# Performance work log

Hardware: AMD Instinct MI355X
Metric: run time of the kernel (lower is better)

Reference implementation:

```python
import jax, jax.numpy as jnp
import numpy as np

B, N, C, H = 2, 2048, 512, 8
D = C // H
SCALE = D ** (-0.5)


def setup_inputs() -> dict:
    key = jax.random.key(0)
    k1, k2, k3 = jax.random.split(key, 3)
    x = jax.random.normal(k1, (B, N, C), dtype=jnp.float32)
    qkv_w = jax.random.normal(k2, (C, 3 * C), dtype=jnp.float32) * (C ** -0.5)
    proj_w = jax.random.normal(k3, (C, C), dtype=jnp.float32) * (C ** -0.5)
    proj_b = jnp.zeros((C,), dtype=jnp.float32)
    return {"x": x, "qkv_w": qkv_w, "proj_w": proj_w, "proj_b": proj_b}


def reference(x, qkv_w, proj_w, proj_b):
    # qkv projection (no bias) -> (B, N, 3, H, D) -> (3, B, H, N, D)
    qkv = jnp.einsum('bnc,cf->bnf', x, qkv_w)
    qkv = qkv.reshape(B, N, 3, H, D).transpose(2, 0, 3, 1, 4)
    q, k, v = qkv[0], qkv[1], qkv[2]
    q = q * SCALE
    attn = jnp.einsum('bhid,bhjd->bhij', q, k)          # (B, H, N, N)
    attn = jax.nn.softmax(attn, axis=-1)
    out = jnp.einsum('bhij,bhjd->bhid', attn, v)         # (B, H, N, D)
    # Faithful to source: reshape (B,H,N,D) -> (B,N,C) WITHOUT transposing
    out = out.reshape(B, N, C)
    out = jnp.einsum('bnc,cd->bnd', out, proj_w) + proj_b
    return out
```

## Files before the change

kernel.cpp:

```cpp
#include <hip/hip_runtime.h>
#include <math.h>

constexpr int Bb = 2;
constexpr int Nn = 2048;
constexpr int Cc = 512;
constexpr int Hh = 8;
constexpr int Dd = 64;

typedef short short8 __attribute__((ext_vector_type(8)));
typedef float floatx4 __attribute__((ext_vector_type(4)));
typedef float floatx16 __attribute__((ext_vector_type(16)));

__device__ inline short8 bcs8(uint4 u) { return __builtin_bit_cast(short8, u); }
__device__ inline float4 bcf4(uint4 u) { return __builtin_bit_cast(float4, u); }

__device__ inline floatx4 mfma16(short8 a, short8 b, floatx4 c) {
    return __builtin_amdgcn_mfma_f32_16x16x32_bf16(a, b, c, 0, 0, 0);
}
__device__ inline floatx16 mfma32(short8 a, short8 b, floatx16 c) {
    return __builtin_amdgcn_mfma_f32_32x32x16_bf16(a, b, c, 0, 0, 0);
}

typedef __attribute__((address_space(1))) void gvoid;
typedef __attribute__((address_space(3))) void svoid;
__device__ inline void glds16(const void* g, void* l) {
    __builtin_amdgcn_global_load_lds((const gvoid*)g, (svoid*)l, 16, 0, 0);
}

#if __has_builtin(__builtin_amdgcn_exp2f)
#define EXP2(x) __builtin_amdgcn_exp2f(x)
#else
#define EXP2(x) __expf((x) * 0.69314718056f)
#endif

__device__ inline unsigned pk_trunc(float a, float b) {
    return __builtin_amdgcn_perm(__float_as_uint(b), __float_as_uint(a), 0x07060302u);
}
__device__ inline unsigned pk_rne(float a, float b) {
    unsigned ua = __float_as_uint(a); ua += 0x7fffu + ((ua >> 16) & 1u);
    unsigned ub = __float_as_uint(b); ub += 0x7fffu + ((ub >> 16) & 1u);
    return __builtin_amdgcn_perm(ub, ua, 0x07060302u);
}
__device__ inline unsigned short rne1(float a) {
    unsigned u = __float_as_uint(a); u += 0x7fffu + ((u >> 16) & 1u);
    return (unsigned short)(u >> 16);
}
__device__ inline float tr16(float a) {
    return __uint_as_float(__float_as_uint(a) & 0xffff0000u);
}
__device__ inline void split8(float4 A, float4 B, uint4& hi, uint4& lo) {
    hi = make_uint4(pk_trunc(A.x, A.y), pk_trunc(A.z, A.w),
                    pk_trunc(B.x, B.y), pk_trunc(B.z, B.w));
    lo = make_uint4(pk_trunc(A.x - tr16(A.x), A.y - tr16(A.y)),
                    pk_trunc(A.z - tr16(A.z), A.w - tr16(A.w)),
                    pk_trunc(B.x - tr16(B.x), B.y - tr16(B.y)),
                    pk_trunc(B.z - tr16(B.z), B.w - tr16(B.w)));
}

__global__ __launch_bounds__(256) void prep(const float* __restrict__ qkv_w,
                                            const float* __restrict__ proj_w,
                                            unsigned short* __restrict__ wqh,
                                            unsigned short* __restrict__ wql,
                                            unsigned short* __restrict__ wph,
                                            unsigned short* __restrict__ wpl)
{
    __shared__ float Tl[64][68];
    int bid = blockIdx.x;
    const float* src; unsigned short *dh, *dlo; int W, f0, k0;
    if (bid < 192) { int kt = bid / 24, ft = bid % 24; W = 1536; src = qkv_w; dh = wqh; dlo = wql; f0 = ft * 64; k0 = kt * 64; }
    else { int b2 = bid - 192; int kt = b2 / 8, ft = b2 % 8; W = 512; src = proj_w; dh = wph; dlo = wpl; f0 = ft * 64; k0 = kt * 64; }
    int t = threadIdx.x;
    {
        int kl = t >> 2, fc = (t & 3) * 16;
        const float* p = src + (size_t)(k0 + kl) * W + f0 + fc;
        #pragma unroll
        for (int i = 0; i < 4; ++i) {
            float4 v = *(const float4*)(p + i * 4);
            Tl[kl][fc + i * 4 + 0] = v.x; Tl[kl][fc + i * 4 + 1] = v.y;
            Tl[kl][fc + i * 4 + 2] = v.z; Tl[kl][fc + i * 4 + 3] = v.w;
        }
    }
    __syncthreads();
    {
        int fl = t >> 2, kc = (t & 3) * 16;
        float v[16];
        #pragma unroll
        for (int i = 0; i < 16; ++i) v[i] = Tl[kc + i][fl];
        unsigned hi[8], lo[8];
        #pragma unroll
        for (int i = 0; i < 8; ++i) {
            float a = v[2 * i], b = v[2 * i + 1];
            hi[i] = pk_trunc(a, b);
            lo[i] = pk_trunc(a - tr16(a), b - tr16(b));
        }
        unsigned short* oh = dh + (size_t)(f0 + fl) * 512 + k0 + kc;
        unsigned short* ol = dlo + (size_t)(f0 + fl) * 512 + k0 + kc;
        *(uint4*)oh = make_uint4(hi[0], hi[1], hi[2], hi[3]);
        *(uint4*)(oh + 8) = make_uint4(hi[4], hi[5], hi[6], hi[7]);
        *(uint4*)ol = make_uint4(lo[0], lo[1], lo[2], lo[3]);
        *(uint4*)(ol + 8) = make_uint4(lo[4], lo[5], lo[6], lo[7]);
    }
}

__global__ __launch_bounds__(256, 3) void gemm_qkv(const float* __restrict__ x,
                                                   const unsigned short* __restrict__ wh,
                                                   const unsigned short* __restrict__ wl,
                                                   unsigned short* __restrict__ qd,
                                                   unsigned short* __restrict__ kfrag,
                                                   unsigned short* __restrict__ vfrag)
{
    __shared__ __align__(16) char smem[49152];
    const int tid = threadIdx.x, lane = tid & 63, w = tid >> 6;
    const int l15 = lane & 15, l4 = lane >> 4;
    const int row0 = blockIdx.y * 128, col0 = blockIdx.x * 64;
    const int wm = w >> 1, wn = w & 1;

    floatx4 acc[4][2];
    #pragma unroll
    for (int i = 0; i < 4; ++i)
        #pragma unroll
        for (int j = 0; j < 2; ++j)
            #pragma unroll
            for (int r = 0; r < 4; ++r) acc[i][j][r] = 0.f;

    auto stage = [&](int k0, char* buf) {
        #pragma unroll
        for (int i = 0; i < 4; ++i) {
            int sid = w * 4 + i; int mt = sid >> 1, sub = sid & 1;
            const float* src = x + (size_t)(row0 + mt * 16 + l15) * 512 + k0 + l4 * 8 + sub * 4;
            glds16(src, buf + sid * 1024);
        }
        #pragma unroll
        for (int i = 0; i < 2; ++i) {
            int sid = w * 2 + i; int nt = sid >> 1, comp = sid & 1;
            const unsigned short* src = (comp ? wl : wh) + (size_t)(col0 + nt * 16 + l15) * 512 + k0 + l4 * 8;
            glds16(src, buf + 16384 + comp * 4096 + nt * 1024);
        }
    };

    stage(0, smem);
    for (int it = 0; it < 16; ++it) {
        __syncthreads();
        char* buf = smem + (it & 1) * 24576;
        if (it < 15) stage((it + 1) * 32, smem + ((it + 1) & 1) * 24576);
        char* Ab = buf; char* Bh = buf + 16384; char* Bl = buf + 20480;
        short8 af[4][2], bf[2][2];
        #pragma unroll
        for (int mt = 0; mt < 4; ++mt) {
            int off = (((wm * 4 + mt) * 2) << 10) + (lane << 4);
            float4 fa = bcf4(*(const uint4*)(Ab + off));
            float4 fb = bcf4(*(const uint4*)(Ab + off + 1024));
            uint4 hi, lo;
            split8(fa, fb, hi, lo);
            af[mt][0] = bcs8(hi);
            af[mt][1] = bcs8(lo);
        }
        #pragma unroll
        for (int nt = 0; nt < 2; ++nt) {
            int off = ((wn * 2 + nt) << 10) + (lane << 4);
            bf[nt][0] = bcs8(*(const uint4*)(Bh + off));
            bf[nt][1] = bcs8(*(const uint4*)(Bl + off));
        }
        #pragma unroll
        for (int mt = 0; mt < 4; ++mt)
            #pragma unroll
            for (int nt = 0; nt < 2; ++nt) {
                acc[mt][nt] = mfma16(af[mt][0], bf[nt][0], acc[mt][nt]);
                acc[mt][nt] = mfma16(af[mt][0], bf[nt][1], acc[mt][nt]);
                acc[mt][nt] = mfma16(af[mt][1], bf[nt][0], acc[mt][nt]);
            }
    }
    #pragma unroll
    for (int mt = 0; mt < 4; ++mt)
        #pragma unroll
        for (int nt = 0; nt < 2; ++nt) {
            int c = col0 + (wn * 2 + nt) * 16 + l15;
            int which = c >> 9;
            int head = (c >> 6) & 7, d = c & 63;
            int tokb = row0 + (wm * 4 + mt) * 16 + l4 * 4;
            int b = tokb >> 11, n = tokb & 2047;
            int bh = b * 8 + head;
            if (which == 0) {
                #pragma unroll
                for (int r = 0; r < 4; ++r)
                    qd[(size_t)(bh * 2048 + n + r) * 64 + d] = rne1(acc[mt][nt][r] * 0.18033688f);
            } else if (which == 1) {
                int s = d >> 4;
                size_t fb_ = ((size_t)(bh * 64 + (n >> 5)) * 4 + s) * 512 + (d & 7);
                int hl = ((d >> 3) & 1) * 32;
                #pragma unroll
                for (int r = 0; r < 4; ++r)
                    kfrag[fb_ + (size_t)(hl + ((n + r) & 31)) * 8] = rne1(acc[mt][nt][r]);
            } else {
                int j = n >> 4, mtv = d >> 5;
                uint2 pv;
                pv.x = pk_rne(acc[mt][nt][0], acc[mt][nt][1]);
                pv.y = pk_rne(acc[mt][nt][2], acc[mt][nt][3]);
                *(uint2*)&vfrag[((size_t)(bh * 128 + j) * 2 + mtv) * 512 +
                                (size_t)(((n >> 3) & 1) * 32 + (d & 31)) * 8 + (n & 7)] = pv;
            }
        }
}

__global__ __launch_bounds__(256, 4) void attn(const unsigned short* __restrict__ qd,
                                               const unsigned short* __restrict__ kfrag,
                                               const unsigned short* __restrict__ vfrag,
                                               unsigned short* __restrict__ Oh,
                                               unsigned short* __restrict__ Ol)
{
    __shared__ float Ms[2048];
    __shared__ float Ls[64];
    __shared__ float Ts[2176];

    int bid = blockIdx.x;
    int xcd = bid & 7; int rr = bid >> 3;
    int qt = rr & 63; int bhi = rr >> 6;
    int bh = (bhi << 3) | xcd;
    int tid = threadIdx.x, lane = tid & 63, kg = tid >> 6;
    int l31 = lane & 31, h = lane >> 5;

    short8 qf[4];
    #pragma unroll
    for (int s = 0; s < 4; ++s)
        qf[s] = bcs8(*(const uint4*)(qd + ((size_t)bh * 2048 + qt * 32 + l31) * 64 + s * 16 + h * 8));

    const uint4 onesu = make_uint4(0x3F803F80u, 0x3F803F80u, 0x3F803F80u, 0x3F803F80u);
    const short8 onesf = bcs8(onesu);

    floatx16 OT[2], OTl;
    #pragma unroll
    for (int i = 0; i < 2; ++i)
        #pragma unroll
        for (int r = 0; r < 16; ++r) OT[i][r] = 0.f;
    #pragma unroll
    for (int r = 0; r < 16; ++r) OTl[r] = 0.f;

    const unsigned short* kb_ = kfrag + ((size_t)(bh * 64 + kg * 16) * 4) * 512 + lane * 8;
    const unsigned short* vb_ = vfrag + ((size_t)(bh * 128 + kg * 32) * 2) * 512 + lane * 8;

    #pragma unroll
    for (int c = 0; c < 16; ++c) {
        uint4 kfu[4];
        #pragma unroll
        for (int s = 0; s < 4; ++s)
            kfu[s] = *(const uint4*)(kb_ + ((size_t)c * 4 + s) * 512);
        uint4 vfu[2][2];
        #pragma unroll
        for (int kc = 0; kc < 2; ++kc)
            #pragma unroll
            for (int mtv = 0; mtv < 2; ++mtv)
                vfu[kc][mtv] = *(const uint4*)(vb_ + ((size_t)(c * 2 + kc) * 2 + mtv) * 512);

        floatx16 st;
        #pragma unroll
        for (int r = 0; r < 16; ++r) st[r] = 0.f;
        #pragma unroll
        for (int s = 0; s < 4; ++s) st = mfma32(bcs8(kfu[s]), qf[s], st);

        unsigned P2[8];
        #pragma unroll
        for (int s2 = 0; s2 < 8; ++s2)
            P2[s2] = pk_trunc(EXP2(st[2 * s2]), EXP2(st[2 * s2 + 1]));

        #pragma unroll
        for (int kc = 0; kc < 2; ++kc) {
            unsigned X0 = P2[4 * kc + 0], X1 = P2[4 * kc + 1];
            unsigned Y0 = P2[4 * kc + 2], Y1 = P2[4 * kc + 3];
            unsigned T0 = h ? X0 : Y0;
            unsigned T1 = h ? X1 : Y1;
            unsigned To0 = __shfl_xor(T0, 32, 64);
            unsigned To1 = __shfl_xor(T1, 32, 64);
            uint4 fu;
            fu.x = h ? To0 : X0;
            fu.y = h ? To1 : X1;
            fu.z = h ? Y0 : To0;
            fu.w = h ? Y1 : To1;
            short8 pf = bcs8(fu);
            OT[0] = mfma32(bcs8(vfu[kc][0]), pf, OT[0]);
            OT[1] = mfma32(bcs8(vfu[kc][1]), pf, OT[1]);
            OTl = mfma32(onesf, pf, OTl);
        }
    }

    if (kg == 3) {
        #pragma unroll
        for (int mtv = 0; mtv < 2; ++mtv)
            #pragma unroll
            for (int r = 0; r < 16; ++r) {
                int d = mtv * 32 + (r & 3) + 8 * (r >> 2) + 4 * h;
                Ms[d * 32 + l31] = OT[mtv][r];
            }
        Ls[h * 32 + l31] = OTl[0];
    }
    __syncthreads();
    if (kg == 2) {
        #pragma unroll
        for (int mtv = 0; mtv < 2; ++mtv)
            #pragma unroll
            for (int r = 0; r < 16; ++r) {
                int d = mtv * 32 + (r & 3) + 8 * (r >> 2) + 4 * h;
                Ms[d * 32 + l31] += OT[mtv][r];
            }
        Ls[h * 32 + l31] += OTl[0];
    }
    __syncthreads();
    if (kg == 1) {
        #pragma unroll
        for (int mtv = 0; mtv < 2; ++mtv)
            #pragma unroll
            for (int r = 0; r < 16; ++r) {
                int d = mtv * 32 + (r & 3) + 8 * (r >> 2) + 4 * h;
                Ms[d * 32 + l31] += OT[mtv][r];
            }
        Ls[h * 32 + l31] += OTl[0];
    }
    __syncthreads();
    if (kg == 0) {
        #pragma unroll
        for (int mtv = 0; mtv < 2; ++mtv)
            #pragma unroll
            for (int r = 0; r < 16; ++r) {
                int d = mtv * 32 + (r & 3) + 8 * (r >> 2) + 4 * h;
                OT[mtv][r] += Ms[d * 32 + l31];
            }
        float inv = 1.f / (Ls[h * 32 + l31] + OTl[0]);
        #pragma unroll
        for (int mtv = 0; mtv < 2; ++mtv)
            #pragma unroll
            for (int r = 0; r < 16; ++r) {
                int d = mtv * 32 + (r & 3) + 8 * (r >> 2) + 4 * h;
                Ts[l31 * 68 + d] = OT[mtv][r] * inv;
            }
    }
    __syncthreads();
    {
        int q = tid >> 3, dc = (tid & 7) * 8;
        float vv[8];
        #pragma unroll
        for (int i = 0; i < 8; ++i) vv[i] = Ts[q * 68 + dc + i];
        unsigned hi[4], lo[4];
        #pragma unroll
        for (int i = 0; i < 4; ++i) {
            float a = vv[2 * i], bb = vv[2 * i + 1];
            hi[i] = pk_trunc(a, bb);
            lo[i] = pk_trunc(a - tr16(a), bb - tr16(bb));
        }
        size_t bo = ((size_t)(bh * 2048 + qt * 32 + q)) * 64 + dc;
        *(uint4*)(Oh + bo) = make_uint4(hi[0], hi[1], hi[2], hi[3]);
        *(uint4*)(Ol + bo) = make_uint4(lo[0], lo[1], lo[2], lo[3]);
    }
}

__global__ __launch_bounds__(256, 2) void gemm_proj(const unsigned short* __restrict__ Ah_g,
                                                    const unsigned short* __restrict__ Al_g,
                                                    const unsigned short* __restrict__ wh,
                                                    const unsigned short* __restrict__ wl,
                                                    const float* __restrict__ bias,
                                                    float* __restrict__ out)
{
    __shared__ __align__(16) char smem[32768];
    const int tid = threadIdx.x, lane = tid & 63, w = tid >> 6;
    const int l15 = lane & 15, l4 = lane >> 4;
    const int row0 = blockIdx.y * 64, col0 = blockIdx.x * 64;
    const int wm = w >> 1, wn = w & 1;

    floatx4 acc[2][2];
    #pragma unroll
    for (int i = 0; i < 2; ++i)
        #pragma unroll
        for (int j = 0; j < 2; ++j)
            #pragma unroll
            for (int r = 0; r < 4; ++r) acc[i][j][r] = 0.f;

    auto stage = [&](int k0, char* buf) {
        #pragma unroll
        for (int i = 0; i < 4; ++i) {
            int sid = w * 4 + i;
            if (sid < 8) {
                int mt = sid >> 1, comp = sid & 1;
                const unsigned short* src = (comp ? Al_g : Ah_g) + (size_t)(row0 + mt * 16 + l15) * 512 + k0 + l4 * 8;
                glds16(src, buf + (comp ? 4096 : 0) + mt * 1024);
            } else {
                int s2 = sid - 8; int nt = s2 >> 1, comp = s2 & 1;
                const unsigned short* src = (comp ? wl : wh) + (size_t)(col0 + nt * 16 + l15) * 512 + k0 + l4 * 8;
                glds16(src, buf + (comp ? 12288 : 8192) + nt * 1024);
            }
        }
    };

    stage(0, smem);
    for (int it = 0; it < 16; ++it) {
        __syncthreads();
        char* buf = smem + (it & 1) * 16384;
        if (it < 15) stage((it + 1) * 32, smem + ((it + 1) & 1) * 16384);
        char* Ah = buf; char* Al = buf + 4096; char* Bh = buf + 8192; char* Bl = buf + 12288;
        short8 af[2][2], bf[2][2];
        #pragma unroll
        for (int mt = 0; mt < 2; ++mt) {
            int off = ((wm * 2 + mt) << 10) + (lane << 4);
            af[mt][0] = bcs8(*(const uint4*)(Ah + off));
            af[mt][1] = bcs8(*(const uint4*)(Al + off));
        }
        #pragma unroll
        for (int nt = 0; nt < 2; ++nt) {
            int off = ((wn * 2 + nt) << 10) + (lane << 4);
            bf[nt][0] = bcs8(*(const uint4*)(Bh + off));
            bf[nt][1] = bcs8(*(const uint4*)(Bl + off));
        }
        #pragma unroll
        for (int mt = 0; mt < 2; ++mt)
            #pragma unroll
            for (int nt = 0; nt < 2; ++nt) {
                acc[mt][nt] = mfma16(af[mt][0], bf[nt][0], acc[mt][nt]);
                acc[mt][nt] = mfma16(af[mt][0], bf[nt][1], acc[mt][nt]);
                acc[mt][nt] = mfma16(af[mt][1], bf[nt][0], acc[mt][nt]);
            }
    }
    #pragma unroll
    for (int mt = 0; mt < 2; ++mt)
        #pragma unroll
        for (int nt = 0; nt < 2; ++nt) {
            int c = col0 + (wn * 2 + nt) * 16 + l15;
            float bv = bias[c];
            #pragma unroll
            for (int r = 0; r < 4; ++r) {
                int tok = row0 + (wm * 2 + mt) * 16 + l4 * 4 + r;
                out[(size_t)tok * 512 + c] = acc[mt][nt][r] + bv;
            }
        }
}

extern "C" void kernel_launch(void* const* d_in, const int* in_sizes, int n_in,
                              void* d_out, int out_size, void* d_ws, size_t ws_size,
                              hipStream_t stream)
{
    const float* x      = (const float*)d_in[0];
    const float* qkv_w  = (const float*)d_in[1];
    const float* proj_w = (const float*)d_in[2];
    const float* proj_b = (const float*)d_in[3];
    float* out = (float*)d_out;

    char* ws = (char*)d_ws;
    unsigned short* qd    = (unsigned short*)ws;
    unsigned short* kfrag = (unsigned short*)(ws + 4194304);
    unsigned short* vfrag = (unsigned short*)(ws + 8388608);
    unsigned short* wqh   = (unsigned short*)(ws + 12582912);
    unsigned short* wql   = (unsigned short*)(ws + 14155776);
    unsigned short* wph   = (unsigned short*)(ws + 15728640);
    unsigned short* wpl   = (unsigned short*)(ws + 16252928);
    unsigned short* Oh    = (unsigned short*)(ws + 16777216);
    unsigned short* Ol    = (unsigned short*)(ws + 20971520);

    prep<<<256, 256, 0, stream>>>(qkv_w, proj_w, wqh, wql, wph, wpl);
    gemm_qkv<<<dim3(24, 32), 256, 0, stream>>>(x, wqh, wql, qd, kfrag, vfrag);
    attn<<<1024, 256, 0, stream>>>(qd, kfrag, vfrag, Oh, Ol);
    gemm_proj<<<dim3(8, 64), 256, 0, stream>>>(Oh, Ol, wph, wpl, proj_b, out);
}
```

Before: 149.9 us.

## Pre-pack GEMM operands into MFMA fragment layout and drop LDS staging

The prep kernel now also splits x into bf16 hi/lo and writes x, both weight matrices, and the attention output into a fragment-major layout that matches the MFMA operand order. The QKV and projection GEMMs then load operands straight from global memory into registers, with no LDS double-buffering and no barriers, and the QKV tile shape changes to 64x128 with higher occupancy. This removes the in-GEMM fp32 split work and the shared-memory traffic and sync. In exchange it adds an extra pass writing x to the workspace and relies on caches for operand reuse across waves instead of LDS.

Result: faster. 139.9 us (-6.7%).

```diff
diff --git a/kernel.cpp b/kernel.cpp
--- a/kernel.cpp
+++ b/kernel.cpp
@@ -12,19 +12,12 @@
 typedef float floatx16 __attribute__((ext_vector_type(16)));
 
 __device__ inline short8 bcs8(uint4 u) { return __builtin_bit_cast(short8, u); }
-__device__ inline float4 bcf4(uint4 u) { return __builtin_bit_cast(float4, u); }
 
 __device__ inline floatx4 mfma16(short8 a, short8 b, floatx4 c) {
     return __builtin_amdgcn_mfma_f32_16x16x32_bf16(a, b, c, 0, 0, 0);
 }
 __device__ inline floatx16 mfma32(short8 a, short8 b, floatx16 c) {
     return __builtin_amdgcn_mfma_f32_32x32x16_bf16(a, b, c, 0, 0, 0);
-}
-
-typedef __attribute__((address_space(1))) void gvoid;
-typedef __attribute__((address_space(3))) void svoid;
-__device__ inline void glds16(const void* g, void* l) {
-    __builtin_amdgcn_global_load_lds((const gvoid*)g, (svoid*)l, 16, 0, 0);
 }
 
 #if __has_builtin(__builtin_amdgcn_exp2f)
@@ -57,19 +50,41 @@
                     pk_trunc(B.z - tr16(B.z), B.w - tr16(B.w)));
 }
 
+
 __global__ __launch_bounds__(256) void prep(const float* __restrict__ qkv_w,
                                             const float* __restrict__ proj_w,
-                                            unsigned short* __restrict__ wqh,
-                                            unsigned short* __restrict__ wql,
-                                            unsigned short* __restrict__ wph,
-                                            unsigned short* __restrict__ wpl)
+                                            const float* __restrict__ x,
+                                            unsigned short* __restrict__ wqfrag,
+                                            unsigned short* __restrict__ wpfrag,
+                                            unsigned short* __restrict__ xfrag)
 {
     __shared__ float Tl[64][68];
     int bid = blockIdx.x;
-    const float* src; unsigned short *dh, *dlo; int W, f0, k0;
-    if (bid < 192) { int kt = bid / 24, ft = bid % 24; W = 1536; src = qkv_w; dh = wqh; dlo = wql; f0 = ft * 64; k0 = kt * 64; }
-    else { int b2 = bid - 192; int kt = b2 / 8, ft = b2 % 8; W = 512; src = proj_w; dh = wph; dlo = wpl; f0 = ft * 64; k0 = kt * 64; }
     int t = threadIdx.x;
+    if (bid >= 256) {
+        int xb = bid - 256;
+        int tok = xb * 16 + (t >> 4);
+        int kc = t & 15;
+        const float* px = x + (size_t)tok * 512 + kc * 32;
+        uint4 h[4], l[4];
+        #pragma unroll
+        for (int o = 0; o < 4; ++o) {
+            float4 fa = *(const float4*)(px + o * 8);
+            float4 fb = *(const float4*)(px + o * 8 + 4);
+            split8(fa, fb, h[o], l[o]);
+        }
+        int mt = tok >> 4, m = tok & 15;
+        unsigned short* fb_ = xfrag + ((size_t)(mt * 16 + kc) * 2) * 512;
+        #pragma unroll
+        for (int o = 0; o < 4; ++o) {
+            *(uint4*)(fb_ + (m + 16 * o) * 8) = h[o];
+            *(uint4*)(fb_ + 512 + (m + 16 * o) * 8) = l[o];
+        }
+        return;
+    }
+    const float* src; unsigned short* dfrag; int W, f0, k0;
+    if (bid < 192) { int kt = bid / 24, ft = bid % 24; W = 1536; src = qkv_w; dfrag = wqfrag; f0 = ft * 64; k0 = kt * 64; }
+    else { int b2 = bid - 192; int kt = b2 / 8, ft = b2 % 8; W = 512; src = proj_w; dfrag = wpfrag; f0 = ft * 64; k0 = kt * 64; }
     {
         int kl = t >> 2, fc = (t & 3) * 16;
         const float* p = src + (size_t)(k0 + kl) * W + f0 + fc;
@@ -82,10 +97,10 @@
     }
     __syncthreads();
     {
-        int fl = t >> 2, kc = (t & 3) * 16;
+        int fl = t >> 2, kc16 = (t & 3) * 16;
         float v[16];
         #pragma unroll
-        for (int i = 0; i < 16; ++i) v[i] = Tl[kc + i][fl];
+        for (int i = 0; i < 16; ++i) v[i] = Tl[kc16 + i][fl];
         unsigned hi[8], lo[8];
         #pragma unroll
         for (int i = 0; i < 8; ++i) {
@@ -93,27 +108,29 @@
             hi[i] = pk_trunc(a, b);
             lo[i] = pk_trunc(a - tr16(a), b - tr16(b));
         }
-        unsigned short* oh = dh + (size_t)(f0 + fl) * 512 + k0 + kc;
-        unsigned short* ol = dlo + (size_t)(f0 + fl) * 512 + k0 + kc;
-        *(uint4*)oh = make_uint4(hi[0], hi[1], hi[2], hi[3]);
-        *(uint4*)(oh + 8) = make_uint4(hi[4], hi[5], hi[6], hi[7]);
-        *(uint4*)ol = make_uint4(lo[0], lo[1], lo[2], lo[3]);
-        *(uint4*)(ol + 8) = make_uint4(lo[4], lo[5], lo[6], lo[7]);
-    }
-}
-
-__global__ __launch_bounds__(256, 3) void gemm_qkv(const float* __restrict__ x,
-                                                   const unsigned short* __restrict__ wh,
-                                                   const unsigned short* __restrict__ wl,
+        int f = f0 + fl;
+        int nt = f >> 4, nin = f & 15;
+        int kc = (k0 + kc16) >> 5;
+        int oct0 = (kc16 >> 3) & 3;
+        unsigned short* fb_ = dfrag + ((size_t)(nt * 16 + kc) * 2) * 512;
+        *(uint4*)(fb_ + (nin + 16 * oct0) * 8) = make_uint4(hi[0], hi[1], hi[2], hi[3]);
+        *(uint4*)(fb_ + (nin + 16 * (oct0 + 1)) * 8) = make_uint4(hi[4], hi[5], hi[6], hi[7]);
+        *(uint4*)(fb_ + 512 + (nin + 16 * oct0) * 8) = make_uint4(lo[0], lo[1], lo[2], lo[3]);
+        *(uint4*)(fb_ + 512 + (nin + 16 * (oct0 + 1)) * 8) = make_uint4(lo[4], lo[5], lo[6], lo[7]);
+    }
+}
+
+__global__ __launch_bounds__(256, 4) void gemm_qkv(const unsigned short* __restrict__ xfrag,
+                                                   const unsigned short* __restrict__ wqfrag,
                                                    unsigned short* __restrict__ qd,
                                                    unsigned short* __restrict__ kfrag,
                                                    unsigned short* __restrict__ vfrag)
 {
-    __shared__ __align__(16) char smem[49152];
     const int tid = threadIdx.x, lane = tid & 63, w = tid >> 6;
     const int l15 = lane & 15, l4 = lane >> 4;
-    const int row0 = blockIdx.y * 128, col0 = blockIdx.x * 64;
-    const int wm = w >> 1, wn = w & 1;
+    const int row0 = blockIdx.y * 64, col0 = blockIdx.x * 128;
+    const int mt0 = row0 >> 4;
+    const int nt0 = (col0 >> 4) + w * 2;
 
     floatx4 acc[4][2];
     #pragma unroll
@@ -123,61 +140,39 @@
             #pragma unroll
             for (int r = 0; r < 4; ++r) acc[i][j][r] = 0.f;
 
-    auto stage = [&](int k0, char* buf) {
-        #pragma unroll
-        for (int i = 0; i < 4; ++i) {
-            int sid = w * 4 + i; int mt = sid >> 1, sub = sid & 1;
-            const float* src = x + (size_t)(row0 + mt * 16 + l15) * 512 + k0 + l4 * 8 + sub * 4;
-            glds16(src, buf + sid * 1024);
-        }
-        #pragma unroll
-        for (int i = 0; i < 2; ++i) {
-            int sid = w * 2 + i; int nt = sid >> 1, comp = sid & 1;
-            const unsigned short* src = (comp ? wl : wh) + (size_t)(col0 + nt * 16 + l15) * 512 + k0 + l4 * 8;
-            glds16(src, buf + 16384 + comp * 4096 + nt * 1024);
-        }
-    };
-
-    stage(0, smem);
-    for (int it = 0; it < 16; ++it) {
-        __syncthreads();
-        char* buf = smem + (it & 1) * 24576;
-        if (it < 15) stage((it + 1) * 32, smem + ((it + 1) & 1) * 24576);
-        char* Ab = buf; char* Bh = buf + 16384; char* Bl = buf + 20480;
-        short8 af[4][2], bf[2][2];
+    const unsigned short* xb = xfrag + (size_t)lane * 8;
+    const unsigned short* wb = wqfrag + (size_t)lane * 8;
+
+    #pragma unroll
+    for (int kc = 0; kc < 16; ++kc) {
+        short8 bf[2][2];
+        #pragma unroll
+        for (int nt = 0; nt < 2; ++nt) {
+            size_t fb_ = ((size_t)((nt0 + nt) * 16 + kc) * 2) * 512;
+            bf[nt][0] = bcs8(*(const uint4*)(wb + fb_));
+            bf[nt][1] = bcs8(*(const uint4*)(wb + fb_ + 512));
+        }
         #pragma unroll
         for (int mt = 0; mt < 4; ++mt) {
-            int off = (((wm * 4 + mt) * 2) << 10) + (lane << 4);
-            float4 fa = bcf4(*(const uint4*)(Ab + off));
-            float4 fb = bcf4(*(const uint4*)(Ab + off + 1024));
-            uint4 hi, lo;
-            split8(fa, fb, hi, lo);
-            af[mt][0] = bcs8(hi);
-            af[mt][1] = bcs8(lo);
-        }
+            size_t fa_ = ((size_t)((mt0 + mt) * 16 + kc) * 2) * 512;
+            short8 ah = bcs8(*(const uint4*)(xb + fa_));
+            short8 al = bcs8(*(const uint4*)(xb + fa_ + 512));
+            #pragma unroll
+            for (int nt = 0; nt < 2; ++nt) {
+                acc[mt][nt] = mfma16(ah, bf[nt][0], acc[mt][nt]);
+                acc[mt][nt] = mfma16(ah, bf[nt][1], acc[mt][nt]);
+                acc[mt][nt] = mfma16(al, bf[nt][0], acc[mt][nt]);
+            }
+        }
+    }
+    #pragma unroll
+    for (int mt = 0; mt < 4; ++mt)
         #pragma unroll
         for (int nt = 0; nt < 2; ++nt) {
-            int off = ((wn * 2 + nt) << 10) + (lane << 4);
-            bf[nt][0] = bcs8(*(const uint4*)(Bh + off));
-            bf[nt][1] = bcs8(*(const uint4*)(Bl + off));
-        }
-        #pragma unroll
-        for (int mt = 0; mt < 4; ++mt)
-            #pragma unroll
-            for (int nt = 0; nt < 2; ++nt) {
-                acc[mt][nt] = mfma16(af[mt][0], bf[nt][0], acc[mt][nt]);
-                acc[mt][nt] = mfma16(af[mt][0], bf[nt][1], acc[mt][nt]);
-                acc[mt][nt] = mfma16(af[mt][1], bf[nt][0], acc[mt][nt]);
-            }
-    }
-    #pragma unroll
-    for (int mt = 0; mt < 4; ++mt)
-        #pragma unroll
-        for (int nt = 0; nt < 2; ++nt) {
-            int c = col0 + (wn * 2 + nt) * 16 + l15;
+            int c = col0 + (w * 2 + nt) * 16 + l15;
             int which = c >> 9;
             int head = (c >> 6) & 7, d = c & 63;
-            int tokb = row0 + (wm * 4 + mt) * 16 + l4 * 4;
+            int tokb = row0 + mt * 16 + l4 * 4;
             int b = tokb >> 11, n = tokb & 2047;
             int bh = b * 8 + head;
             if (which == 0) {
@@ -205,8 +200,7 @@
 __global__ __launch_bounds__(256, 4) void attn(const unsigned short* __restrict__ qd,
                                                const unsigned short* __restrict__ kfrag,
                                                const unsigned short* __restrict__ vfrag,
-                                               unsigned short* __restrict__ Oh,
-                                               unsigned short* __restrict__ Ol)
+                                               unsigned short* __restrict__ Ofrag)
 {
     __shared__ float Ms[2048];
     __shared__ float Ls[64];
@@ -345,24 +339,27 @@
             hi[i] = pk_trunc(a, bb);
             lo[i] = pk_trunc(a - tr16(a), bb - tr16(bb));
         }
-        size_t bo = ((size_t)(bh * 2048 + qt * 32 + q)) * 64 + dc;
-        *(uint4*)(Oh + bo) = make_uint4(hi[0], hi[1], hi[2], hi[3]);
-        *(uint4*)(Ol + bo) = make_uint4(lo[0], lo[1], lo[2], lo[3]);
-    }
-}
-
-__global__ __launch_bounds__(256, 2) void gemm_proj(const unsigned short* __restrict__ Ah_g,
-                                                    const unsigned short* __restrict__ Al_g,
-                                                    const unsigned short* __restrict__ wh,
-                                                    const unsigned short* __restrict__ wl,
+        int ng = qt * 32 + q;
+        int r = bh * 256 + (ng >> 3);
+        int cc = (ng & 7) * 64 + dc;
+        int mt = r >> 4, m = r & 15, kc = cc >> 5, oct = (cc >> 3) & 3;
+        unsigned short* fb_ = Ofrag + ((size_t)(mt * 16 + kc) * 2) * 512 + (m + 16 * oct) * 8;
+        *(uint4*)fb_ = make_uint4(hi[0], hi[1], hi[2], hi[3]);
+        *(uint4*)(fb_ + 512) = make_uint4(lo[0], lo[1], lo[2], lo[3]);
+    }
+}
+
+__global__ __launch_bounds__(256, 4) void gemm_proj(const unsigned short* __restrict__ Ofrag,
+                                                    const unsigned short* __restrict__ wpfrag,
                                                     const float* __restrict__ bias,
                                                     float* __restrict__ out)
 {
-    __shared__ __align__(16) char smem[32768];
     const int tid = threadIdx.x, lane = tid & 63, w = tid >> 6;
     const int l15 = lane & 15, l4 = lane >> 4;
     const int row0 = blockIdx.y * 64, col0 = blockIdx.x * 64;
     const int wm = w >> 1, wn = w & 1;
+    const int mt0 = (row0 >> 4) + wm * 2;
+    const int nt0 = (col0 >> 4) + wn * 2;
 
     floatx4 acc[2][2];
     #pragma unroll
@@ -372,59 +369,40 @@
             #pragma unroll
             for (int r = 0; r < 4; ++r) acc[i][j][r] = 0.f;
 
-    auto stage = [&](int k0, char* buf) {
-        #pragma unroll
-        for (int i = 0; i < 4; ++i) {
-            int sid = w * 4 + i;
-            if (sid < 8) {
-                int mt = sid >> 1, comp = sid & 1;
-                const unsigned short* src = (comp ? Al_g : Ah_g) + (size_t)(row0 + mt * 16 + l15) * 512 + k0 + l4 * 8;
-                glds16(src, buf + (comp ? 4096 : 0) + mt * 1024);
-            } else {
-                int s2 = sid - 8; int nt = s2 >> 1, comp = s2 & 1;
-                const unsigned short* src = (comp ? wl : wh) + (size_t)(col0 + nt * 16 + l15) * 512 + k0 + l4 * 8;
-                glds16(src, buf + (comp ? 12288 : 8192) + nt * 1024);
-            }
-        }
-    };
-
-    stage(0, smem);
-    for (int it = 0; it < 16; ++it) {
-        __syncthreads();
-        char* buf = smem + (it & 1) * 16384;
-        if (it < 15) stage((it + 1) * 32, smem + ((it + 1) & 1) * 16384);
-        char* Ah = buf; char* Al = buf + 4096; char* Bh = buf + 8192; char* Bl = buf + 12288;
-        short8 af[2][2], bf[2][2];
+    const unsigned short* ab = Ofrag + (size_t)lane * 8;
+    const unsigned short* wb = wpfrag + (size_t)lane * 8;
+
+    #pragma unroll
+    for (int kc = 0; kc < 16; ++kc) {
+        short8 bf[2][2];
+        #pragma unroll
+        for (int nt = 0; nt < 2; ++nt) {
+            size_t fb_ = ((size_t)((nt0 + nt) * 16 + kc) * 2) * 512;
+            bf[nt][0] = bcs8(*(const uint4*)(wb + fb_));
+            bf[nt][1] = bcs8(*(const uint4*)(wb + fb_ + 512));
+        }
         #pragma unroll
         for (int mt = 0; mt < 2; ++mt) {
-            int off = ((wm * 2 + mt) << 10) + (lane << 4);
-            af[mt][0] = bcs8(*(const uint4*)(Ah + off));
-            af[mt][1] = bcs8(*(const uint4*)(Al + off));
-        }
+            size_t fa_ = ((size_t)((mt0 + mt) * 16 + kc) * 2) * 512;
+            short8 ah = bcs8(*(const uint4*)(ab + fa_));
+            short8 al = bcs8(*(const uint4*)(ab + fa_ + 512));
+            #pragma unroll
+            for (int nt = 0; nt < 2; ++nt) {
+                acc[mt][nt] = mfma16(ah, bf[nt][0], acc[mt][nt]);
+                acc[mt][nt] = mfma16(ah, bf[nt][1], acc[mt][nt]);
+                acc[mt][nt] = mfma16(al, bf[nt][0], acc[mt][nt]);
+            }
+        }
+    }
+    #pragma unroll
+    for (int mt = 0; mt < 2; ++mt)
         #pragma unroll
         for (int nt = 0; nt < 2; ++nt) {
-            int off = ((wn * 2 + nt) << 10) + (lane << 4);
-            bf[nt][0] = bcs8(*(const uint4*)(Bh + off));
-            bf[nt][1] = bcs8(*(const uint4*)(Bl + off));
-        }
-        #pragma unroll
-        for (int mt = 0; mt < 2; ++mt)
-            #pragma unroll
-            for (int nt = 0; nt < 2; ++nt) {
-                acc[mt][nt] = mfma16(af[mt][0], bf[nt][0], acc[mt][nt]);
-                acc[mt][nt] = mfma16(af[mt][0], bf[nt][1], acc[mt][nt]);
-                acc[mt][nt] = mfma16(af[mt][1], bf[nt][0], acc[mt][nt]);
-            }
-    }
-    #pragma unroll
-    for (int mt = 0; mt < 2; ++mt)
-        #pragma unroll
-        for (int nt = 0; nt < 2; ++nt) {
-            int c = col0 + (wn * 2 + nt) * 16 + l15;
+            int c = col0 + wn * 32 + nt * 16 + l15;
             float bv = bias[c];
             #pragma unroll
             for (int r = 0; r < 4; ++r) {
-                int tok = row0 + (wm * 2 + mt) * 16 + l4 * 4 + r;
+                int tok = row0 + wm * 32 + mt * 16 + l4 * 4 + r;
                 out[(size_t)tok * 512 + c] = acc[mt][nt][r] + bv;
             }
         }
@@ -441,18 +419,16 @@
     float* out = (float*)d_out;
 
     char* ws = (char*)d_ws;
-    unsigned short* qd    = (unsigned short*)ws;
-    unsigned short* kfrag = (unsigned short*)(ws + 4194304);
-    unsigned short* vfrag = (unsigned short*)(ws + 8388608);
-    unsigned short* wqh   = (unsigned short*)(ws + 12582912);
-    unsigned short* wql   = (unsigned short*)(ws + 14155776);
-    unsigned short* wph   = (unsigned short*)(ws + 15728640);
-    unsigned short* wpl   = (unsigned short*)(ws + 16252928);
-    unsigned short* Oh    = (unsigned short*)(ws + 16777216);
-    unsigned short* Ol    = (unsigned short*)(ws + 20971520);
-
-    prep<<<256, 256, 0, stream>>>(qkv_w, proj_w, wqh, wql, wph, wpl);
-    gemm_qkv<<<dim3(24, 32), 256, 0, stream>>>(x, wqh, wql, qd, kfrag, vfrag);
-    attn<<<1024, 256, 0, stream>>>(qd, kfrag, vfrag, Oh, Ol);
-    gemm_proj<<<dim3(8, 64), 256, 0, stream>>>(Oh, Ol, wph, wpl, proj_b, out);
-}
+    unsigned short* xfrag  = (unsigned short*)ws;
+    unsigned short* wqfrag = (unsigned short*)(ws + 8388608);
+    unsigned short* wpfrag = (unsigned short*)(ws + 11534336);
+    unsigned short* qd     = (unsigned short*)(ws + 12582912);
+    unsigned short* kfrag  = (unsigned short*)(ws + 16777216);
+    unsigned short* vfrag  = (unsigned short*)(ws + 20971520);
+    unsigned short* Ofrag  = (unsigned short*)(ws + 25165824);
+
+    prep<<<512, 256, 0, stream>>>(qkv_w, proj_w, x, wqfrag, wpfrag, xfrag);
+    gemm_qkv<<<dim3(12, 64), 256, 0, stream>>>(xfrag, wqfrag, qd, kfrag, vfrag);
+    attn<<<1024, 256, 0, stream>>>(qd, kfrag, vfrag, Ofrag);
+    gemm_proj<<<dim3(8, 64), 256, 0, stream>>>(Ofrag, wpfrag, proj_b, out);
+}
```
